# Kernel tuning notes

Hardware: AMD Instinct MI355X
Metric: run time of the kernel (lower is better)

The kernel has to match this reference:

```python
import jax, jax.numpy as jnp
import numpy as np

B, S, D, H = 8, 1024, 1024, 16
HD = D // H  # head dim = 64

def setup_inputs() -> dict:
    key = jax.random.key(0)
    ks = jax.random.split(key, 7)
    scale = 1.0 / np.sqrt(HD)
    return {
        "sequences": jax.random.normal(ks[0], (B, S, D), dtype=jnp.float32),
        "Wq": jax.random.normal(ks[1], (H, HD, HD), dtype=jnp.float32) * scale,
        "bq": jax.random.normal(ks[2], (H, HD), dtype=jnp.float32) * scale,
        "Wk": jax.random.normal(ks[3], (H, HD, HD), dtype=jnp.float32) * scale,
        "bk": jax.random.normal(ks[4], (H, HD), dtype=jnp.float32) * scale,
        "Wv": jax.random.normal(ks[5], (H, HD, HD), dtype=jnp.float32) * scale,
        "bv": jax.random.normal(ks[6], (H, HD), dtype=jnp.float32) * scale,
    }

def reference(sequences, Wq, bq, Wk, bk, Wv, bv):
    # split hidden dim into heads: [B, S, H, HD]
    x = sequences.reshape(B, S, H, HD)
    # per-head Linear: y = x @ W^T + b  (torch nn.Linear convention)
    q = jnp.einsum('bshd,hed->bshe', x, Wq) + bq  # [B,S,H,HD]
    k = jnp.einsum('bshd,hed->bshe', x, Wk) + bk
    v = jnp.einsum('bshd,hed->bshe', x, Wv) + bv
    # scaled dot-product attention per head
    dots = jnp.einsum('bqhe,bkhe->bhqk', q, k) / jnp.sqrt(jnp.float32(HD))
    attn = jax.nn.softmax(dots, axis=-1)  # [B,H,S,S]
    out = jnp.einsum('bhqk,bkhe->bqhe', attn, v)  # [B,S,H,HD]
    # hstack of per-head results == concat along last dim
    return out.reshape(B, S, D)
```

## Files before the change

kernel.cpp:

```cpp
#include <hip/hip_runtime.h>
#include <hip/hip_bf16.h>

typedef unsigned short u16;
typedef __attribute__((ext_vector_type(8))) short bf16x8;
typedef __attribute__((ext_vector_type(4))) float f32x4;
typedef __attribute__((ext_vector_type(16))) float f32x16;

#define LOG2E 1.44269504088896f

__device__ __forceinline__ unsigned cvtpk(float lo, float hi_) {
  unsigned r;
  asm("v_cvt_pk_bf16_f32 %0, %1, %2" : "=v"(r) : "v"(lo), "v"(hi_));
  return r;
}
__device__ __forceinline__ bf16x8 pack8(float4 a, float4 b) {
  union { unsigned wd[4]; bf16x8 v; } u;
  u.wd[0] = cvtpk(a.x, a.y); u.wd[1] = cvtpk(a.z, a.w);
  u.wd[2] = cvtpk(b.x, b.y); u.wd[3] = cvtpk(b.z, b.w);
  return u.v;
}

__global__ __launch_bounds__(256) void qkv_proj_kernel(
    const float* __restrict__ x,
    const float* __restrict__ Wq, const float* __restrict__ bq,
    const float* __restrict__ Wk, const float* __restrict__ bk,
    const float* __restrict__ Wv, const float* __restrict__ bv,
    u16* __restrict__ qws, u16* __restrict__ kws, u16* __restrict__ vtws)
{
  constexpr int S = 1024, D = 1024, H = 16;
  const int tid  = threadIdx.x;
  const int lane = tid & 63;
  const int w    = tid >> 6;
  const int st   = blockIdx.x, h = blockIdx.y, b = blockIdx.z;
  const int s0   = st * 128;
  const int col  = lane & 15, lhi = lane >> 4;
  const int tok0 = w * 32;
  const size_t bh = (size_t)b * H + h;
  const int swz  = (col & 7) << 4;

  bf16x8 xf[2][2];
#pragma unroll
  for (int tt = 0; tt < 2; ++tt)
#pragma unroll
    for (int ks = 0; ks < 2; ++ks) {
      const float* xp = x + ((size_t)b * S + s0 + tok0 + tt * 16 + col) * D
                        + h * 64 + ks * 32 + lhi * 8;
      xf[tt][ks] = pack8(*(const float4*)xp, *(const float4*)(xp + 4));
    }

#pragma unroll
  for (int o = 0; o < 3; ++o) {
    const float* Wh = ((o == 0) ? Wq : (o == 1) ? Wk : Wv) + (size_t)h * 4096;
    const float* bp = ((o == 0) ? bq : (o == 1) ? bk : bv) + h * 64;

    bf16x8 wf[4][2];
#pragma unroll
    for (int et = 0; et < 4; ++et)
#pragma unroll
      for (int ks = 0; ks < 2; ++ks) {
        const float* wp = Wh + (et * 16 + col) * 64 + ks * 32 + lhi * 8;
        wf[et][ks] = pack8(*(const float4*)wp, *(const float4*)(wp + 4));
      }

    f32x4 acc[2][4];
#pragma unroll
    for (int tt = 0; tt < 2; ++tt)
#pragma unroll
      for (int et = 0; et < 4; ++et) acc[tt][et] = f32x4{0.f, 0.f, 0.f, 0.f};

    if (o < 2) {
#pragma unroll
      for (int et = 0; et < 4; ++et)
#pragma unroll
        for (int ks = 0; ks < 2; ++ks) {
          acc[0][et] = __builtin_amdgcn_mfma_f32_16x16x32_bf16(wf[et][ks], xf[0][ks], acc[0][et], 0, 0, 0);
          acc[1][et] = __builtin_amdgcn_mfma_f32_16x16x32_bf16(wf[et][ks], xf[1][ks], acc[1][et], 0, 0, 0);
        }
      const float mul = (o == 0) ? (0.125f * LOG2E) : 1.0f;
#pragma unroll
      for (int et = 0; et < 4; ++et) {
        const float4 bb = *(const float4*)(bp + et * 16 + lhi * 4);
#pragma unroll
        for (int tt = 0; tt < 2; ++tt) {
          const float v0 = (acc[tt][et][0] + bb.x) * mul;
          const float v1 = (acc[tt][et][1] + bb.y) * mul;
          const float v2 = (acc[tt][et][2] + bb.z) * mul;
          const float v3 = (acc[tt][et][3] + bb.w) * mul;
          uint2 r; r.x = cvtpk(v0, v1); r.y = cvtpk(v2, v3);
          const int token = s0 + tok0 + tt * 16 + col;
          if (o == 0) {
            *(uint2*)(qws + (bh * S + token) * 64 + et * 16 + lhi * 4) = r;
          } else {
            const int rim = token & 63, kb = token >> 6;
            const int byt = (et * 32 + lhi * 8) ^ swz;
            *(uint2*)(kws + (bh * 16 + kb) * 4096 + rim * 64 + (byt >> 1)) = r;
          }
        }
      }
    } else {
#pragma unroll
      for (int et = 0; et < 4; ++et)
#pragma unroll
        for (int ks = 0; ks < 2; ++ks) {
          acc[0][et] = __builtin_amdgcn_mfma_f32_16x16x32_bf16(xf[0][ks], wf[et][ks], acc[0][et], 0, 0, 0);
          acc[1][et] = __builtin_amdgcn_mfma_f32_16x16x32_bf16(xf[1][ks], wf[et][ks], acc[1][et], 0, 0, 0);
        }
#pragma unroll
      for (int et = 0; et < 4; ++et) {
        const float be = bp[et * 16 + col];
        const int e = et * 16 + col;
#pragma unroll
        for (int tt = 0; tt < 2; ++tt) {
          uint2 r;
          r.x = cvtpk(acc[tt][et][0] + be, acc[tt][et][1] + be);
          r.y = cvtpk(acc[tt][et][2] + be, acc[tt][et][3] + be);
          const int token = s0 + tok0 + tt * 16 + lhi * 4;
          const int kb = token >> 6;
          const int m  = (token & 63) >> 2;
          const int icb = ((m >> 2) << 4) | ((m & 1) << 3) | (((m >> 1) & 1) << 2);
          const int byt = (icb * 2) ^ swz;
          *(uint2*)(vtws + (bh * 16 + kb) * 4096 + e * 64 + (byt >> 1)) = r;
        }
      }
    }
  }
}

__global__ __launch_bounds__(256) void attn_kernel(
    const u16* __restrict__ qws, const u16* __restrict__ kws,
    const u16* __restrict__ vtws, float* __restrict__ out)
{
  constexpr int S = 1024, D = 1024, H = 16;
  const int tid  = threadIdx.x;
  const int lane = tid & 63;
  const int w    = tid >> 6;
  const int id   = blockIdx.x;
  const int qb   = id >> 7;
  const int bhid = id & 127;
  const int b    = bhid >> 4;
  const int h    = bhid & 15;
  const int ql   = lane & 31;
  const int hi   = lane >> 5;

  __shared__ u16 kbuf[2 * 4096];
  __shared__ u16 vbuf[2 * 4096];

  const size_t bh = (size_t)b * H + h;
  const int qrow0 = qb * 128 + w * 32;
  const u16* qbase = qws + (bh * S + qrow0) * 64;
  const u16* kimg0 = kws + bh * 16 * 4096;
  const u16* vimg0 = vtws + bh * 16 * 4096;

  bf16x8 qf[4];
#pragma unroll
  for (int dc = 0; dc < 4; ++dc)
    qf[dc] = *(const bf16x8*)(qbase + ql * 64 + dc * 16 + hi * 8);

  f32x16 oa0, oa1;
#pragma unroll
  for (int r = 0; r < 16; ++r) { oa0[r] = 0.f; oa1[r] = 0.f; }
  float lrow = 0.f;

  auto stage = [&](int buf, int kb) {
    const u16* kimg = kimg0 + kb * 4096;
    const u16* vimg = vimg0 + kb * 4096;
#pragma unroll
    for (int i = 0; i < 2; ++i) {
      const int chunk = w + i * 4;
      __builtin_amdgcn_global_load_lds(
          (const __attribute__((address_space(1))) unsigned int*)(kimg + chunk * 512 + lane * 8),
          (__attribute__((address_space(3))) unsigned int*)(&kbuf[buf * 4096 + chunk * 512]),
          16, 0, 0);
      __builtin_amdgcn_global_load_lds(
          (const __attribute__((address_space(1))) unsigned int*)(vimg + chunk * 512 + lane * 8),
          (__attribute__((address_space(3))) unsigned int*)(&vbuf[buf * 4096 + chunk * 512]),
          16, 0, 0);
    }
  };

  stage(0, 0);
  __syncthreads();

  const int swz = ((ql & 7) << 4);
  int cur = 0;
  for (int kb = 0; kb < 16; ++kb) {
    if (kb < 15) stage(cur ^ 1, kb + 1);

    const u16* kp = &kbuf[cur * 4096];
    f32x16 sa0, sa1;
#pragma unroll
    for (int r = 0; r < 16; ++r) { sa0[r] = 0.f; sa1[r] = 0.f; }
    __builtin_amdgcn_s_setprio(1);
#pragma unroll
    for (int dc = 0; dc < 4; ++dc) {
      const int c = ((dc * 32 + hi * 16) ^ swz) >> 1;
      const bf16x8 k0 = *(const bf16x8*)(kp + ql * 64 + c);
      const bf16x8 k1 = *(const bf16x8*)(kp + (32 + ql) * 64 + c);
      sa0 = __builtin_amdgcn_mfma_f32_32x32x16_bf16(k0, qf[dc], sa0, 0, 0, 0);
      sa1 = __builtin_amdgcn_mfma_f32_32x32x16_bf16(k1, qf[dc], sa1, 0, 0, 0);
    }
    __builtin_amdgcn_s_setprio(0);

    float s0 = 0.f, s1 = 0.f, s2 = 0.f, s3 = 0.f;
#pragma unroll
    for (int r = 0; r < 16; r += 4) {
      sa0[r]     = __builtin_amdgcn_exp2f(sa0[r]);     s0 += sa0[r];
      sa0[r + 1] = __builtin_amdgcn_exp2f(sa0[r + 1]); s1 += sa0[r + 1];
      sa0[r + 2] = __builtin_amdgcn_exp2f(sa0[r + 2]); s2 += sa0[r + 2];
      sa0[r + 3] = __builtin_amdgcn_exp2f(sa0[r + 3]); s3 += sa0[r + 3];
      sa1[r]     = __builtin_amdgcn_exp2f(sa1[r]);     s0 += sa1[r];
      sa1[r + 1] = __builtin_amdgcn_exp2f(sa1[r + 1]); s1 += sa1[r + 1];
      sa1[r + 2] = __builtin_amdgcn_exp2f(sa1[r + 2]); s2 += sa1[r + 2];
      sa1[r + 3] = __builtin_amdgcn_exp2f(sa1[r + 3]); s3 += sa1[r + 3];
    }
    float rs = (s0 + s1) + (s2 + s3);
    rs += __shfl_xor(rs, 32);
    lrow += rs;

    bf16x8 pf[4];
#pragma unroll
    for (int ks = 0; ks < 4; ++ks) {
      const f32x16& s_ = (ks < 2) ? sa0 : sa1;
      const int base = (ks & 1) * 8;
      union { unsigned wd[4]; bf16x8 hv; } pu;
      pu.wd[0] = cvtpk(s_[base + 0], s_[base + 1]);
      pu.wd[1] = cvtpk(s_[base + 2], s_[base + 3]);
      pu.wd[2] = cvtpk(s_[base + 4], s_[base + 5]);
      pu.wd[3] = cvtpk(s_[base + 6], s_[base + 7]);
      pf[ks] = pu.hv;
    }

    const u16* vp = &vbuf[cur * 4096];
    __builtin_amdgcn_s_setprio(1);
#pragma unroll
    for (int ks = 0; ks < 4; ++ks) {
      const int cv = ((ks * 32 + hi * 16) ^ swz) >> 1;
      const bf16x8 v0 = *(const bf16x8*)(vp + ql * 64 + cv);
      const bf16x8 v1 = *(const bf16x8*)(vp + (32 + ql) * 64 + cv);
      oa0 = __builtin_amdgcn_mfma_f32_32x32x16_bf16(v0, pf[ks], oa0, 0, 0, 0);
      oa1 = __builtin_amdgcn_mfma_f32_32x32x16_bf16(v1, pf[ks], oa1, 0, 0, 0);
    }
    __builtin_amdgcn_s_setprio(0);

    __syncthreads();
    cur ^= 1;
  }

  const float inv = 1.0f / lrow;
  float* op = out + ((size_t)b * S + qrow0 + ql) * D + h * 64;
#pragma unroll
  for (int rr = 0; rr < 4; ++rr) {
    float4 v;
    v.x = oa0[rr * 4 + 0] * inv; v.y = oa0[rr * 4 + 1] * inv;
    v.z = oa0[rr * 4 + 2] * inv; v.w = oa0[rr * 4 + 3] * inv;
    *(float4*)(op + rr * 8 + hi * 4) = v;
    float4 u;
    u.x = oa1[rr * 4 + 0] * inv; u.y = oa1[rr * 4 + 1] * inv;
    u.z = oa1[rr * 4 + 2] * inv; u.w = oa1[rr * 4 + 3] * inv;
    *(float4*)(op + 32 + rr * 8 + hi * 4) = u;
  }
}

extern "C" void kernel_launch(void* const* d_in, const int* in_sizes, int n_in,
                              void* d_out, int out_size, void* d_ws, size_t ws_size,
                              hipStream_t stream)
{
  const float* x  = (const float*)d_in[0];
  const float* Wq = (const float*)d_in[1];
  const float* bq = (const float*)d_in[2];
  const float* Wk = (const float*)d_in[3];
  const float* bk = (const float*)d_in[4];
  const float* Wv = (const float*)d_in[5];
  const float* bv = (const float*)d_in[6];
  float* out = (float*)d_out;

  u16* qws  = (u16*)d_ws;
  u16* kws  = qws + (size_t)8 * 16 * 1024 * 64;
  u16* vtws = kws + (size_t)8 * 16 * 1024 * 64;

  dim3 blk(256);
  dim3 grid1(8, 16, 8);
  hipLaunchKernelGGL(qkv_proj_kernel, grid1, blk, 0, stream,
                     x, Wq, bq, Wk, bk, Wv, bv, qws, kws, vtws);
  dim3 grid2(1024);
  hipLaunchKernelGGL(attn_kernel, grid2, blk, 0, stream,
                     qws, kws, vtws, out);
}
```

Measured before the change: 169.8 us.

## Load K and V fragments directly from global memory instead of LDS staging

Removes the double-buffered LDS staging of K and V tiles (global_load_lds plus a barrier every iteration). Each wave now reads its K and V MFMA fragments straight from global memory into registers, and the XOR swizzle in the projection kernel's K/V layout is dropped to match. This removes barriers and LDS traffic, but the four waves of a block redundantly fetch the same K/V from global/L2. It also loses the prefetch overlap and raises register pressure.

```diff
diff --git a/kernel.cpp b/kernel.cpp
--- a/kernel.cpp
+++ b/kernel.cpp
@@ -36,7 +36,6 @@
   const int col  = lane & 15, lhi = lane >> 4;
   const int tok0 = w * 32;
   const size_t bh = (size_t)b * H + h;
-  const int swz  = (col & 7) << 4;
 
   bf16x8 xf[2][2];
 #pragma unroll
@@ -92,8 +91,7 @@
             *(uint2*)(qws + (bh * S + token) * 64 + et * 16 + lhi * 4) = r;
           } else {
             const int rim = token & 63, kb = token >> 6;
-            const int byt = (et * 32 + lhi * 8) ^ swz;
-            *(uint2*)(kws + (bh * 16 + kb) * 4096 + rim * 64 + (byt >> 1)) = r;
+            *(uint2*)(kws + (bh * 16 + kb) * 4096 + rim * 64 + et * 16 + lhi * 4) = r;
           }
         }
       }
@@ -118,8 +116,7 @@
           const int kb = token >> 6;
           const int m  = (token & 63) >> 2;
           const int icb = ((m >> 2) << 4) | ((m & 1) << 3) | (((m >> 1) & 1) << 2);
-          const int byt = (icb * 2) ^ swz;
-          *(uint2*)(vtws + (bh * 16 + kb) * 4096 + e * 64 + (byt >> 1)) = r;
+          *(uint2*)(vtws + (bh * 16 + kb) * 4096 + e * 64 + icb) = r;
         }
       }
     }
@@ -142,14 +139,9 @@
   const int ql   = lane & 31;
   const int hi   = lane >> 5;
 
-  __shared__ u16 kbuf[2 * 4096];
-  __shared__ u16 vbuf[2 * 4096];
-
   const size_t bh = (size_t)b * H + h;
   const int qrow0 = qb * 128 + w * 32;
   const u16* qbase = qws + (bh * S + qrow0) * 64;
-  const u16* kimg0 = kws + bh * 16 * 4096;
-  const u16* vimg0 = vtws + bh * 16 * 4096;
 
   bf16x8 qf[4];
 #pragma unroll
@@ -161,45 +153,37 @@
   for (int r = 0; r < 16; ++r) { oa0[r] = 0.f; oa1[r] = 0.f; }
   float lrow = 0.f;
 
-  auto stage = [&](int buf, int kb) {
-    const u16* kimg = kimg0 + kb * 4096;
-    const u16* vimg = vimg0 + kb * 4096;
-#pragma unroll
-    for (int i = 0; i < 2; ++i) {
-      const int chunk = w + i * 4;
-      __builtin_amdgcn_global_load_lds(
-          (const __attribute__((address_space(1))) unsigned int*)(kimg + chunk * 512 + lane * 8),
-          (__attribute__((address_space(3))) unsigned int*)(&kbuf[buf * 4096 + chunk * 512]),
-          16, 0, 0);
-      __builtin_amdgcn_global_load_lds(
-          (const __attribute__((address_space(1))) unsigned int*)(vimg + chunk * 512 + lane * 8),
-          (__attribute__((address_space(3))) unsigned int*)(&vbuf[buf * 4096 + chunk * 512]),
-          16, 0, 0);
-    }
-  };
-
-  stage(0, 0);
-  __syncthreads();
-
-  const int swz = ((ql & 7) << 4);
-  int cur = 0;
+  const u16* kp0 = kws  + bh * 16 * 4096 + ql * 64 + hi * 8;
+  const u16* vp0 = vtws + bh * 16 * 4096 + ql * 64 + hi * 8;
+
+#pragma unroll 1
   for (int kb = 0; kb < 16; ++kb) {
-    if (kb < 15) stage(cur ^ 1, kb + 1);
-
-    const u16* kp = &kbuf[cur * 4096];
+    const u16* kp = kp0 + kb * 4096;
+    bf16x8 kf[8];
+#pragma unroll
+    for (int dc = 0; dc < 4; ++dc) {
+      kf[dc]     = *(const bf16x8*)(kp + dc * 16);
+      kf[4 + dc] = *(const bf16x8*)(kp + 2048 + dc * 16);
+    }
+
     f32x16 sa0, sa1;
 #pragma unroll
     for (int r = 0; r < 16; ++r) { sa0[r] = 0.f; sa1[r] = 0.f; }
     __builtin_amdgcn_s_setprio(1);
 #pragma unroll
     for (int dc = 0; dc < 4; ++dc) {
-      const int c = ((dc * 32 + hi * 16) ^ swz) >> 1;
-      const bf16x8 k0 = *(const bf16x8*)(kp + ql * 64 + c);
-      const bf16x8 k1 = *(const bf16x8*)(kp + (32 + ql) * 64 + c);
-      sa0 = __builtin_amdgcn_mfma_f32_32x32x16_bf16(k0, qf[dc], sa0, 0, 0, 0);
-      sa1 = __builtin_amdgcn_mfma_f32_32x32x16_bf16(k1, qf[dc], sa1, 0, 0, 0);
+      sa0 = __builtin_amdgcn_mfma_f32_32x32x16_bf16(kf[dc],     qf[dc], sa0, 0, 0, 0);
+      sa1 = __builtin_amdgcn_mfma_f32_32x32x16_bf16(kf[4 + dc], qf[dc], sa1, 0, 0, 0);
     }
     __builtin_amdgcn_s_setprio(0);
+
+    const u16* vp = vp0 + kb * 4096;
+    bf16x8 vf[8];
+#pragma unroll
+    for (int ks = 0; ks < 4; ++ks) {
+      vf[ks]     = *(const bf16x8*)(vp + ks * 16);
+      vf[4 + ks] = *(const bf16x8*)(vp + 2048 + ks * 16);
+    }
 
     float s0 = 0.f, s1 = 0.f, s2 = 0.f, s3 = 0.f;
 #pragma unroll
@@ -230,20 +214,13 @@
       pf[ks] = pu.hv;
     }
 
-    const u16* vp = &vbuf[cur * 4096];
     __builtin_amdgcn_s_setprio(1);
 #pragma unroll
     for (int ks = 0; ks < 4; ++ks) {
-      const int cv = ((ks * 32 + hi * 16) ^ swz) >> 1;
-      const bf16x8 v0 = *(const bf16x8*)(vp + ql * 64 + cv);
-      const bf16x8 v1 = *(const bf16x8*)(vp + (32 + ql) * 64 + cv);
-      oa0 = __builtin_amdgcn_mfma_f32_32x32x16_bf16(v0, pf[ks], oa0, 0, 0, 0);
-      oa1 = __builtin_amdgcn_mfma_f32_32x32x16_bf16(v1, pf[ks], oa1, 0, 0, 0);
+      oa0 = __builtin_amdgcn_mfma_f32_32x32x16_bf16(vf[ks],     pf[ks], oa0, 0, 0, 0);
+      oa1 = __builtin_amdgcn_mfma_f32_32x32x16_bf16(vf[4 + ks], pf[ks], oa1, 0, 0, 0);
     }
     __builtin_amdgcn_s_setprio(0);
-
-    __syncthreads();
-    cur ^= 1;
   }
 
   const float inv = 1.0f / lrow;
```

Measured after the change: 237.1 us. +39.6%, slower.
